# Performance work log

Measured on AMD Instinct MI355X. Metric: run time of the kernel, lower is better.

## Reference

```python
import jax, jax.numpy as jnp
import numpy as np
from jax import lax

EPS = 1e-12

def _l2norm(v, axis):
    n = jnp.linalg.norm(v, axis=axis, keepdims=True)
    return v / jnp.maximum(n, EPS)

def setup_inputs() -> dict:
    key = jax.random.key(0)
    k1, k2, k3 = jax.random.split(key, 3)
    C, H, W, K = 512, 192, 192, 64
    x = jax.random.normal(k1, (C, H, W), dtype=jnp.float32)
    conv_w = jax.random.normal(k2, (K, C), dtype=jnp.float32) * 0.05  # 1x1 conv, no bias (vladv2=False)
    centroids = jax.random.uniform(k3, (K, C), dtype=jnp.float32)
    return {"x": x, "conv_w": conv_w, "centroids": centroids}

def reference(x, conv_w, centroids):
    K = conv_w.shape[0]
    x4 = x[None]                      # [1,C,H,W]
    N, C, H, W = x4.shape
    L = H * W
    # descriptor-wise L2 normalization over channels
    x4 = _l2norm(x4, axis=1)
    # 1x1 conv -> soft assignment over clusters
    logits = jnp.einsum('kc,nchw->nkhw', conv_w, x4)
    soft = jax.nn.softmax(logits, axis=1)          # [N,K,H,W]
    sa_flat = soft.reshape(N, K, L)
    # top-2 cluster indices per location (argmax + second largest)
    _, top2 = lax.top_k(sa_flat.transpose(0, 2, 1), 2)  # [N,L,2]
    first, second = top2[..., 0], top2[..., 1]
    # unfold 3x3, padding 1: windows [N, L, K, 9] in (kh,kw) order
    pad = jnp.pad(soft, ((0, 0), (0, 0), (1, 1), (1, 1)))
    patches = jnp.stack([pad[:, :, di:di + H, dj:dj + W]
                         for di in range(3) for dj in range(3)], axis=2)  # [N,K,9,H,W]
    windows = patches.reshape(N, K, 9, L).transpose(0, 3, 1, 2)           # [N,L,K,9]
    # keep only windows of the top-2 clusters at each location
    karange = jnp.arange(K)[None, None, :]
    keep = (karange == first[:, :, None]) | (karange == second[:, :, None])  # [N,L,K]
    wsel = windows * keep[..., None].astype(windows.dtype)
    # fold (transpose of unfold): overlap-add back to [N,K,H,W]
    ws = wsel.transpose(0, 2, 3, 1).reshape(N, K, 9, H, W)
    out_pad = jnp.zeros((N, K, H + 2, W + 2), dtype=ws.dtype)
    t = 0
    for di in range(3):
        for dj in range(3):
            out_pad = out_pad.at[:, :, di:di + H, dj:dj + W].add(ws[:, :, t])
            t += 1
    weight = out_pad[:, :, 1:H + 1, 1:W + 1]
    # border mask: (min distance to border)^4
    ii = jnp.arange(H); jj = jnp.arange(W)
    mi = jnp.minimum(H - 1 - ii, ii)[:, None]
    mj = jnp.minimum(W - 1 - jj, jj)[None, :]
    m = jnp.minimum(mi, mj).astype(weight.dtype)
    m2 = m * m
    mask = m2 * m2
    weight = weight * mask[None, None]
    sa2 = weight.reshape(N, K, L)
    # per-cluster residual accumulation, vectorized (replaces the 64-iter loop)
    xf = x4.reshape(N, C, L)
    vlad = jnp.einsum('nkl,ncl->nkc', sa2, xf) - sa2.sum(-1)[..., None] * centroids[None]
    vlad = _l2norm(vlad, axis=2)               # intra-normalization
    v = vlad.reshape(N, -1)
    v = _l2norm(v, axis=1)
    return v
```

## Files before the change

kernel.cpp:

```cpp
#include <hip/hip_runtime.h>

#define HH 192
#define WW 192
#define LL (HH * WW)
#define CC 512
#define KK 64
#define EPSF 1e-12f
typedef unsigned long long ull;
typedef unsigned int uint;
typedef unsigned short ushort;

#define NCHUNK 192
#define CHUNKL (LL / NCHUNK)

typedef short bf16x8 __attribute__((ext_vector_type(8)));
typedef float f32x4 __attribute__((ext_vector_type(4)));

__global__ __launch_bounds__(256) void k0_transpose(const float* __restrict__ w,
                                                    float* __restrict__ wT,
                                                    float* __restrict__ Szero) {
    int idx = blockIdx.x * 256 + threadIdx.x;
    int k = idx >> 9;
    int c = idx & 511;
    wT[c * KK + k] = w[idx];
    if (blockIdx.x == 0 && threadIdx.x < 128) Szero[threadIdx.x] = 0.f;
}

__global__ __launch_bounds__(512) void k1_logits(const float* __restrict__ x,
                                                 const float* __restrict__ wT,
                                                 float* __restrict__ soft,
                                                 float* __restrict__ invn,
                                                 ull* __restrict__ keep) {
    __shared__ float accs[4][16][64];
    __shared__ float sss[64];
    __shared__ float sm1[4][64], sm2[4][64], ssum[4][64], sinv[64];
    __shared__ int   si1[4][64], si2[4][64];
    int t = threadIdx.x, lane = t & 63, wid = t >> 6;
    int l0 = blockIdx.x * 64;
    int kg = __builtin_amdgcn_readfirstlane((wid & 3) * 16);
    int ch = __builtin_amdgcn_readfirstlane((wid >> 2) * 256);

    const float* __restrict__ xcol = x + l0 + lane;

    float acc[16];
#pragma unroll
    for (int q = 0; q < 16; ++q) acc[q] = 0.f;
    float ss = 0.f;

    float xp[16], xn[16];
#pragma unroll
    for (int q = 0; q < 16; ++q) xp[q] = xcol[(size_t)(ch + q) * LL];

    for (int cb = ch; cb < ch + 256; cb += 16) {
        if (cb + 16 < ch + 256) {
#pragma unroll
            for (int q = 0; q < 16; ++q) xn[q] = xcol[(size_t)(cb + 16 + q) * LL];
        }
#pragma unroll
        for (int cc = 0; cc < 16; ++cc) {
            float xv = xp[cc];
            ss = fmaf(xv, xv, ss);
            const float* wr = wT + (size_t)(cb + cc) * KK + kg;
#pragma unroll
            for (int q = 0; q < 16; ++q) acc[q] = fmaf(wr[q], xv, acc[q]);
        }
        if (cb + 16 < ch + 256) {
#pragma unroll
            for (int q = 0; q < 16; ++q) xp[q] = xn[q];
        }
    }

    if (wid >= 4) {
        int w = wid - 4;
#pragma unroll
        for (int q = 0; q < 16; ++q) accs[w][q][lane] = acc[q];
        if (wid == 4) sss[lane] = ss;
    }
    __syncthreads();
    if (wid < 4) {
#pragma unroll
        for (int q = 0; q < 16; ++q) acc[q] += accs[wid][q][lane];
    }
    if (wid == 0) {
        ss += sss[lane];
        float iv = 1.0f / fmaxf(sqrtf(ss), EPSF);
        sinv[lane] = iv;
        invn[l0 + lane] = iv;
    }
    __syncthreads();
    float iv = sinv[lane];

    if (wid < 4) {
        float m1 = -3.0e38f, m2 = -3.0e38f; int i1 = 0, i2 = 0;
#pragma unroll
        for (int q = 0; q < 16; ++q) {
            float lg = acc[q] * iv;
            acc[q] = lg;
            if (lg > m1)      { m2 = m1; i2 = i1; m1 = lg; i1 = kg + q; }
            else if (lg > m2) { m2 = lg; i2 = kg + q; }
        }
        sm1[wid][lane] = m1; si1[wid][lane] = i1;
        sm2[wid][lane] = m2; si2[wid][lane] = i2;
    }
    __syncthreads();

    float M1 = -3.0e38f, M2 = -3.0e38f; int I1 = 0, I2 = 0;
    if (wid < 4) {
#pragma unroll
        for (int w2 = 0; w2 < 4; ++w2) {
            float a1 = sm1[w2][lane]; int b1 = si1[w2][lane];
            float a2 = sm2[w2][lane]; int b2 = si2[w2][lane];
            if (a1 > M1 || (a1 == M1 && b1 < I1)) { M2 = M1; I2 = I1; M1 = a1; I1 = b1; }
            else if (a1 > M2 || (a1 == M2 && b1 < I2)) { M2 = a1; I2 = b1; }
            if (a2 > M1 || (a2 == M1 && b2 < I1)) { M2 = M1; I2 = I1; M1 = a2; I1 = b2; }
            else if (a2 > M2 || (a2 == M2 && b2 < I2)) { M2 = a2; I2 = b2; }
        }
        float es = 0.f;
#pragma unroll
        for (int q = 0; q < 16; ++q) { float e = __expf(acc[q] - M1); acc[q] = e; es += e; }
        ssum[wid][lane] = es;
    }
    __syncthreads();
    if (wid < 4) {
        float St = ssum[0][lane] + ssum[1][lane] + ssum[2][lane] + ssum[3][lane];
        float rs = 1.0f / St;
        float4* sp = (float4*)(soft + (size_t)(l0 + lane) * KK + kg);
#pragma unroll
        for (int q4 = 0; q4 < 4; ++q4) {
            float4 v; v.x = acc[q4*4+0]*rs; v.y = acc[q4*4+1]*rs;
                      v.z = acc[q4*4+2]*rs; v.w = acc[q4*4+3]*rs;
            sp[q4] = v;
        }
        if (wid == 0) keep[l0 + lane] = (1ull << I1) | (1ull << I2);
    }
}

__global__ __launch_bounds__(256) void k2_weight(float* __restrict__ soft,
                                                 const ull* __restrict__ keep,
                                                 const float* __restrict__ invn,
                                                 float* __restrict__ S) {
    __shared__ float sred[4][64];
    int t = threadIdx.x, lane = t & 63, wid = t >> 6;
    int l0 = blockIdx.x * 32 + wid * 8;
    float sk = 0.f;
#pragma unroll
    for (int p = 0; p < 8; ++p) {
        int l = l0 + p;
        int i = l / WW, j = l % WW;
        int m = min(min(i, HH - 1 - i), min(j, WW - 1 - j));
        float bm = (float)m; bm *= bm; bm *= bm;
        int cnt = 0;
#pragma unroll
        for (int di = -1; di <= 1; ++di) {
            int ii = i + di;
            if (ii < 0 || ii >= HH) continue;
#pragma unroll
            for (int dj = -1; dj <= 1; ++dj) {
                int jj = j + dj;
                if (jj < 0 || jj >= WW) continue;
                ull nb = keep[ii * WW + jj];
                cnt += (int)((nb >> lane) & 1ull);
            }
        }
        float v = soft[(size_t)l * KK + lane];
        float u = v * (float)cnt * bm;
        sk += u;
        soft[(size_t)l * KK + lane] = u * invn[l];
    }
    sred[wid][lane] = sk;
    __syncthreads();
    if (wid == 0)
        atomicAdd(&S[lane], sred[0][lane] + sred[1][lane] + sred[2][lane] + sred[3][lane]);
}

__device__ inline void cvt_pair(float v0, float v1, uint& hp, uint& lp) {
    uint b0 = __float_as_uint(v0), b1 = __float_as_uint(v1);
    uint h0 = b0 & 0xFFFF0000u, h1 = b1 & 0xFFFF0000u;
    float r0 = v0 - __uint_as_float(h0);
    float r1 = v1 - __uint_as_float(h1);
    hp = (h0 >> 16) | h1;
    lp = (__float_as_uint(r0) >> 16) | (__float_as_uint(r1) & 0xFFFF0000u);
}

__global__ __launch_bounds__(256) void k3_mfma(const float* __restrict__ w2,
                                               const float* __restrict__ x,
                                               float* __restrict__ partials) {
    __shared__ ushort wa_hi[64][40], wa_lo[64][40];
    __shared__ ushort xb_hi[128][40], xb_lo[128][40];
    int chunk = blockIdx.x;
    int c0 = blockIdx.y * 128;
    int l0 = chunk * CHUNKL;
    int t = threadIdx.x, lane = t & 63, wid = t >> 6;
    int m = lane & 15, quad = lane >> 4;

    f32x4 acc[4][2];
#pragma unroll
    for (int kg = 0; kg < 4; ++kg)
#pragma unroll
        for (int cg = 0; cg < 2; ++cg) acc[kg][cg] = (f32x4){0.f, 0.f, 0.f, 0.f};

    for (int lb = 0; lb < CHUNKL; lb += 32) {
        {
            int k = t & 63, rg = t >> 6;
#pragma unroll
            for (int i = 0; i < 4; ++i) {
                int lp = rg + 4 * i;
                int gl = l0 + lb + 2 * lp;
                float v0 = w2[(size_t)gl * KK + k];
                float v1 = w2[(size_t)(gl + 1) * KK + k];
                uint hp, lq;
                cvt_pair(v0, v1, hp, lq);
                *(uint*)&wa_hi[k][2 * lp] = hp;
                *(uint*)&wa_lo[k][2 * lp] = lq;
            }
        }
        {
            int lp = t & 15, cb = t >> 4;
            int gl = l0 + lb + 2 * lp;
#pragma unroll
            for (int i = 0; i < 8; ++i) {
                int c = cb + 16 * i;
                float v0 = x[(size_t)(c0 + c) * LL + gl];
                float v1 = x[(size_t)(c0 + c) * LL + gl + 1];
                uint hp, lq;
                cvt_pair(v0, v1, hp, lq);
                *(uint*)&xb_hi[c][2 * lp] = hp;
                *(uint*)&xb_lo[c][2 * lp] = lq;
            }
        }
        __syncthreads();
        bf16x8 Ah[4], Al[4];
#pragma unroll
        for (int kg = 0; kg < 4; ++kg) {
            Ah[kg] = *(bf16x8*)&wa_hi[kg * 16 + m][quad * 8];
            Al[kg] = *(bf16x8*)&wa_lo[kg * 16 + m][quad * 8];
        }
#pragma unroll
        for (int cg = 0; cg < 2; ++cg) {
            int crow = wid * 32 + cg * 16 + m;
            bf16x8 Bh = *(bf16x8*)&xb_hi[crow][quad * 8];
            bf16x8 Bl = *(bf16x8*)&xb_lo[crow][quad * 8];
#pragma unroll
            for (int kg = 0; kg < 4; ++kg) {
                acc[kg][cg] = __builtin_amdgcn_mfma_f32_16x16x32_bf16(Ah[kg], Bh, acc[kg][cg], 0, 0, 0);
                acc[kg][cg] = __builtin_amdgcn_mfma_f32_16x16x32_bf16(Ah[kg], Bl, acc[kg][cg], 0, 0, 0);
                acc[kg][cg] = __builtin_amdgcn_mfma_f32_16x16x32_bf16(Al[kg], Bh, acc[kg][cg], 0, 0, 0);
            }
        }
        __syncthreads();
    }
    float* pp = partials + (size_t)chunk * KK * CC;
#pragma unroll
    for (int kg = 0; kg < 4; ++kg)
#pragma unroll
        for (int cg = 0; cg < 2; ++cg) {
            int cout = c0 + wid * 32 + cg * 16 + m;
#pragma unroll
            for (int r = 0; r < 4; ++r) {
                int kout = kg * 16 + quad * 4 + r;
                pp[(size_t)kout * CC + cout] = acc[kg][cg][r];
            }
        }
}

__global__ __launch_bounds__(512) void k4a_reduce(const float* __restrict__ partials,
                                                  const float* __restrict__ S,
                                                  const float* __restrict__ cent,
                                                  float* __restrict__ vlad,
                                                  float* __restrict__ rowsq) {
    __shared__ float red[512];
    int k = blockIdx.x;
    int ci = threadIdx.x & 127;
    int c = blockIdx.y * 128 + ci;
    int q = threadIdx.x >> 7;
    const float* pk = partials + (size_t)q * (NCHUNK / 4) * KK * CC + (size_t)k * CC + c;
    float s0 = 0.f, s1 = 0.f, s2 = 0.f, s3 = 0.f;
    for (int ch = 0; ch < NCHUNK / 4; ch += 4) {
        s0 += pk[(size_t)(ch + 0) * KK * CC];
        s1 += pk[(size_t)(ch + 1) * KK * CC];
        s2 += pk[(size_t)(ch + 2) * KK * CC];
        s3 += pk[(size_t)(ch + 3) * KK * CC];
    }
    red[threadIdx.x] = (s0 + s1) + (s2 + s3);
    __syncthreads();
    float vsq = 0.f;
    if (q == 0) {
        float v = red[ci] + red[ci + 128] + red[ci + 256] + red[ci + 384];
        v -= S[k] * cent[k * CC + c];
        vlad[k * CC + c] = v;
        vsq = v * v;
    }
    __syncthreads();
    red[threadIdx.x] = vsq;
    __syncthreads();
    for (int off = 256; off > 0; off >>= 1) {
        if (threadIdx.x < off) red[threadIdx.x] += red[threadIdx.x + off];
        __syncthreads();
    }
    if (threadIdx.x == 0) atomicAdd(&rowsq[k], red[0]);
}

__global__ __launch_bounds__(256) void k4c_finish(const float* __restrict__ vlad,
                                                  const float* __restrict__ rowsq,
                                                  float* __restrict__ out) {
    __shared__ float rns[64];
    int t = threadIdx.x;
    if (t < 64) {
        float tot = rowsq[t];
        float r = 1.0f / fmaxf(sqrtf(tot), EPSF);
        float contrib = tot * r * r;
#pragma unroll
        for (int off = 32; off; off >>= 1) contrib += __shfl_xor(contrib, off, 64);
        float ginv = 1.0f / fmaxf(sqrtf(contrib), EPSF);
        rns[t] = r * ginv;
    }
    __syncthreads();
    int idx4 = blockIdx.x * 256 + t;
    int k = idx4 >> 7;
    float s = rns[k];
    float4 v = ((const float4*)vlad)[idx4];
    v.x *= s; v.y *= s; v.z *= s; v.w *= s;
    ((float4*)out)[idx4] = v;
}

extern "C" void kernel_launch(void* const* d_in, const int* in_sizes, int n_in,
                              void* d_out, int out_size, void* d_ws, size_t ws_size,
                              hipStream_t stream) {
    const float* x      = (const float*)d_in[0];
    const float* conv_w = (const float*)d_in[1];
    const float* cent   = (const float*)d_in[2];
    float* out = (float*)d_out;

    float* ws    = (float*)d_ws;
    float* wT    = ws;
    float* soft  = wT + 32768;
    float* invn  = soft + (size_t)KK * LL;
    float* S     = invn + LL;
    float* rowsq = S + KK;
    float* vlad  = rowsq + KK;
    ull*   keep  = (ull*)(vlad + 32768);
    float* partials = (float*)(keep + LL);

    k0_transpose<<<(KK * CC) / 256, 256, 0, stream>>>(conv_w, wT, S);
    k1_logits<<<LL / 64, 512, 0, stream>>>(x, wT, soft, invn, keep);
    k2_weight<<<LL / 32, 256, 0, stream>>>(soft, keep, invn, S);
    k3_mfma<<<dim3(NCHUNK, 4), 256, 0, stream>>>(soft, x, partials);
    k4a_reduce<<<dim3(KK, 4), 512, 0, stream>>>(partials, S, cent, vlad, rowsq);
    k4c_finish<<<(KK * CC / 4) / 256, 256, 0, stream>>>(vlad, rowsq, out);
}
```

Before: 209.5 us.

## Compute logits with split-bf16 MFMA instead of scalar FP32 FMAs

Rewrites the logits kernel to use 16x16x32 bf16 MFMA instructions, splitting both the weights and x into three bf16 pieces and using six cross products to approximate FP32 accuracy. The weight prep kernel now pre-splits and reorders conv weights into an MFMA fragment layout. Top-2 selection, the norm and the softmax reductions now use cross-lane shuffles instead of shared memory with block syncs. This replaces a scalar-FMA-bound phase with matrix-core work, at the cost of extra split arithmetic on x and a small precision risk that could change top-2 tie outcomes.

```diff
diff --git a/kernel.cpp b/kernel.cpp
--- a/kernel.cpp
+++ b/kernel.cpp
@@ -16,122 +16,145 @@
 typedef short bf16x8 __attribute__((ext_vector_type(8)));
 typedef float f32x4 __attribute__((ext_vector_type(4)));
 
-__global__ __launch_bounds__(256) void k0_transpose(const float* __restrict__ w,
-                                                    float* __restrict__ wT,
-                                                    float* __restrict__ Szero) {
+__device__ inline void split3(float v, ushort& h, ushort& md, ushort& lo) {
+    uint b  = __float_as_uint(v);
+    uint hb = b & 0xFFFF0000u;
+    float r1 = v - __uint_as_float(hb);
+    uint mb = __float_as_uint(r1) & 0xFFFF0000u;
+    float r2 = r1 - __uint_as_float(mb);
+    uint lb = __float_as_uint(r2) & 0xFFFF0000u;
+    h = (ushort)(hb >> 16); md = (ushort)(mb >> 16); lo = (ushort)(lb >> 16);
+}
+
+__global__ __launch_bounds__(256) void k0_prep(const float* __restrict__ w,
+                                               ushort* __restrict__ Whi,
+                                               ushort* __restrict__ Wmid,
+                                               ushort* __restrict__ Wlo,
+                                               float* __restrict__ Szero) {
     int idx = blockIdx.x * 256 + threadIdx.x;
     int k = idx >> 9;
     int c = idx & 511;
-    wT[c * KK + k] = w[idx];
+    int s = c >> 5, w32 = c & 31, quad = w32 >> 3, j = w32 & 7;
+    int kg = k >> 4, m = k & 15;
+    int dst = (((s * 4 + kg) * 4 + quad) * 16 + m) * 8 + j;
+    float v = w[idx];
+    ushort h, md, lo;
+    split3(v, h, md, lo);
+    Whi[dst] = h; Wmid[dst] = md; Wlo[dst] = lo;
     if (blockIdx.x == 0 && threadIdx.x < 128) Szero[threadIdx.x] = 0.f;
 }
 
-__global__ __launch_bounds__(512) void k1_logits(const float* __restrict__ x,
-                                                 const float* __restrict__ wT,
+__global__ __launch_bounds__(128) void k1_logits(const float* __restrict__ x,
+                                                 const ushort* __restrict__ Whi,
+                                                 const ushort* __restrict__ Wmid,
+                                                 const ushort* __restrict__ Wlo,
                                                  float* __restrict__ soft,
                                                  float* __restrict__ invn,
                                                  ull* __restrict__ keep) {
-    __shared__ float accs[4][16][64];
-    __shared__ float sss[64];
-    __shared__ float sm1[4][64], sm2[4][64], ssum[4][64], sinv[64];
-    __shared__ int   si1[4][64], si2[4][64];
     int t = threadIdx.x, lane = t & 63, wid = t >> 6;
-    int l0 = blockIdx.x * 64;
-    int kg = __builtin_amdgcn_readfirstlane((wid & 3) * 16);
-    int ch = __builtin_amdgcn_readfirstlane((wid >> 2) * 256);
-
-    const float* __restrict__ xcol = x + l0 + lane;
-
-    float acc[16];
-#pragma unroll
-    for (int q = 0; q < 16; ++q) acc[q] = 0.f;
-    float ss = 0.f;
-
-    float xp[16], xn[16];
-#pragma unroll
-    for (int q = 0; q < 16; ++q) xp[q] = xcol[(size_t)(ch + q) * LL];
-
-    for (int cb = ch; cb < ch + 256; cb += 16) {
-        if (cb + 16 < ch + 256) {
-#pragma unroll
-            for (int q = 0; q < 16; ++q) xn[q] = xcol[(size_t)(cb + 16 + q) * LL];
-        }
-#pragma unroll
-        for (int cc = 0; cc < 16; ++cc) {
-            float xv = xp[cc];
-            ss = fmaf(xv, xv, ss);
-            const float* wr = wT + (size_t)(cb + cc) * KK + kg;
-#pragma unroll
-            for (int q = 0; q < 16; ++q) acc[q] = fmaf(wr[q], xv, acc[q]);
-        }
-        if (cb + 16 < ch + 256) {
-#pragma unroll
-            for (int q = 0; q < 16; ++q) xp[q] = xn[q];
-        }
-    }
-
-    if (wid >= 4) {
-        int w = wid - 4;
-#pragma unroll
-        for (int q = 0; q < 16; ++q) accs[w][q][lane] = acc[q];
-        if (wid == 4) sss[lane] = ss;
-    }
-    __syncthreads();
-    if (wid < 4) {
-#pragma unroll
-        for (int q = 0; q < 16; ++q) acc[q] += accs[wid][q][lane];
-    }
-    if (wid == 0) {
-        ss += sss[lane];
-        float iv = 1.0f / fmaxf(sqrtf(ss), EPSF);
-        sinv[lane] = iv;
-        invn[l0 + lane] = iv;
-    }
-    __syncthreads();
-    float iv = sinv[lane];
-
-    if (wid < 4) {
-        float m1 = -3.0e38f, m2 = -3.0e38f; int i1 = 0, i2 = 0;
-#pragma unroll
-        for (int q = 0; q < 16; ++q) {
-            float lg = acc[q] * iv;
-            acc[q] = lg;
-            if (lg > m1)      { m2 = m1; i2 = i1; m1 = lg; i1 = kg + q; }
-            else if (lg > m2) { m2 = lg; i2 = kg + q; }
-        }
-        sm1[wid][lane] = m1; si1[wid][lane] = i1;
-        sm2[wid][lane] = m2; si2[wid][lane] = i2;
-    }
-    __syncthreads();
-
-    float M1 = -3.0e38f, M2 = -3.0e38f; int I1 = 0, I2 = 0;
-    if (wid < 4) {
-#pragma unroll
-        for (int w2 = 0; w2 < 4; ++w2) {
-            float a1 = sm1[w2][lane]; int b1 = si1[w2][lane];
-            float a2 = sm2[w2][lane]; int b2 = si2[w2][lane];
+    int m = lane & 15, quad = lane >> 4;
+    int pb = blockIdx.x * 64 + wid * 32;
+
+    f32x4 acc[4][2];
+#pragma unroll
+    for (int kg = 0; kg < 4; ++kg)
+#pragma unroll
+        for (int cg = 0; cg < 2; ++cg) acc[kg][cg] = (f32x4){0.f, 0.f, 0.f, 0.f};
+    float ssA[2] = {0.f, 0.f};
+
+    const float* xq = x + (size_t)(quad * 8) * LL + pb + m;
+
+    for (int s = 0; s < 16; ++s) {
+        bf16x8 Ah[4], Am[4], Al[4];
+#pragma unroll
+        for (int kg = 0; kg < 4; ++kg) {
+            size_t off = (size_t)(((s * 4 + kg) * 64 + lane) * 8);
+            Ah[kg] = *(const bf16x8*)(Whi  + off);
+            Am[kg] = *(const bf16x8*)(Wmid + off);
+            Al[kg] = *(const bf16x8*)(Wlo  + off);
+        }
+        float xv[2][8];
+#pragma unroll
+        for (int j = 0; j < 8; ++j) {
+            const float* xr = xq + (size_t)j * LL;
+            xv[0][j] = xr[0];
+            xv[1][j] = xr[16];
+        }
+        xq += (size_t)32 * LL;
+        bf16x8 Bh[2], Bm[2], Bl[2];
+#pragma unroll
+        for (int cg = 0; cg < 2; ++cg)
+#pragma unroll
+            for (int j = 0; j < 8; ++j) {
+                float v = xv[cg][j];
+                ssA[cg] = fmaf(v, v, ssA[cg]);
+                ushort h, md, lo;
+                split3(v, h, md, lo);
+                Bh[cg][j] = (short)h; Bm[cg][j] = (short)md; Bl[cg][j] = (short)lo;
+            }
+#pragma unroll
+        for (int kg = 0; kg < 4; ++kg)
+#pragma unroll
+            for (int cg = 0; cg < 2; ++cg) {
+                f32x4 a = acc[kg][cg];
+                a = __builtin_amdgcn_mfma_f32_16x16x32_bf16(Ah[kg], Bh[cg], a, 0, 0, 0);
+                a = __builtin_amdgcn_mfma_f32_16x16x32_bf16(Ah[kg], Bm[cg], a, 0, 0, 0);
+                a = __builtin_amdgcn_mfma_f32_16x16x32_bf16(Am[kg], Bh[cg], a, 0, 0, 0);
+                a = __builtin_amdgcn_mfma_f32_16x16x32_bf16(Ah[kg], Bl[cg], a, 0, 0, 0);
+                a = __builtin_amdgcn_mfma_f32_16x16x32_bf16(Al[kg], Bh[cg], a, 0, 0, 0);
+                a = __builtin_amdgcn_mfma_f32_16x16x32_bf16(Am[kg], Bm[cg], a, 0, 0, 0);
+                acc[kg][cg] = a;
+            }
+    }
+
+#pragma unroll
+    for (int cg = 0; cg < 2; ++cg) {
+        float ssv = ssA[cg];
+        ssv += __shfl_xor(ssv, 16);
+        ssv += __shfl_xor(ssv, 32);
+        float iv = 1.0f / fmaxf(sqrtf(ssv), EPSF);
+        int px = pb + cg * 16 + m;
+        if (quad == 0) invn[px] = iv;
+
+        float lg[16];
+        float M1 = -3.0e38f, M2 = -3.0e38f; int I1 = 0, I2 = 0;
+#pragma unroll
+        for (int kg = 0; kg < 4; ++kg)
+#pragma unroll
+            for (int r = 0; r < 4; ++r) {
+                float v = acc[kg][cg][r] * iv;
+                lg[kg * 4 + r] = v;
+                int kk = kg * 16 + quad * 4 + r;
+                if (v > M1)      { M2 = M1; I2 = I1; M1 = v; I1 = kk; }
+                else if (v > M2) { M2 = v; I2 = kk; }
+            }
+#pragma unroll
+        for (int st = 0; st < 2; ++st) {
+            int d = 16 << st;
+            float a1 = __shfl_xor(M1, d); int b1 = __shfl_xor(I1, d);
+            float a2 = __shfl_xor(M2, d); int b2 = __shfl_xor(I2, d);
             if (a1 > M1 || (a1 == M1 && b1 < I1)) { M2 = M1; I2 = I1; M1 = a1; I1 = b1; }
             else if (a1 > M2 || (a1 == M2 && b1 < I2)) { M2 = a1; I2 = b1; }
             if (a2 > M1 || (a2 == M1 && b2 < I1)) { M2 = M1; I2 = I1; M1 = a2; I1 = b2; }
             else if (a2 > M2 || (a2 == M2 && b2 < I2)) { M2 = a2; I2 = b2; }
         }
+
         float es = 0.f;
 #pragma unroll
-        for (int q = 0; q < 16; ++q) { float e = __expf(acc[q] - M1); acc[q] = e; es += e; }
-        ssum[wid][lane] = es;
-    }
-    __syncthreads();
-    if (wid < 4) {
-        float St = ssum[0][lane] + ssum[1][lane] + ssum[2][lane] + ssum[3][lane];
-        float rs = 1.0f / St;
-        float4* sp = (float4*)(soft + (size_t)(l0 + lane) * KK + kg);
-#pragma unroll
-        for (int q4 = 0; q4 < 4; ++q4) {
-            float4 v; v.x = acc[q4*4+0]*rs; v.y = acc[q4*4+1]*rs;
-                      v.z = acc[q4*4+2]*rs; v.w = acc[q4*4+3]*rs;
-            sp[q4] = v;
-        }
-        if (wid == 0) keep[l0 + lane] = (1ull << I1) | (1ull << I2);
+        for (int q = 0; q < 16; ++q) { float e = __expf(lg[q] - M1); lg[q] = e; es += e; }
+        es += __shfl_xor(es, 16);
+        es += __shfl_xor(es, 32);
+        float rs = 1.0f / es;
+
+        float4* sp = (float4*)(soft + (size_t)px * KK + quad * 4);
+#pragma unroll
+        for (int kg = 0; kg < 4; ++kg) {
+            float4 o;
+            o.x = lg[kg * 4 + 0] * rs; o.y = lg[kg * 4 + 1] * rs;
+            o.z = lg[kg * 4 + 2] * rs; o.w = lg[kg * 4 + 3] * rs;
+            sp[kg * 4] = o;
+        }
+        if (quad == 0) keep[px] = (1ull << I1) | (1ull << I2);
     }
 }
 
@@ -332,8 +355,10 @@
     float* out = (float*)d_out;
 
     float* ws    = (float*)d_ws;
-    float* wT    = ws;
-    float* soft  = wT + 32768;
+    ushort* Whi  = (ushort*)ws;
+    ushort* Wmid = Whi + 32768;
+    ushort* Wlo  = Wmid + 32768;
+    float* soft  = ws + 49152;
     float* invn  = soft + (size_t)KK * LL;
     float* S     = invn + LL;
     float* rowsq = S + KK;
@@ -341,8 +366,8 @@
     ull*   keep  = (ull*)(vlad + 32768);
     float* partials = (float*)(keep + LL);
 
-    k0_transpose<<<(KK * CC) / 256, 256, 0, stream>>>(conv_w, wT, S);
-    k1_logits<<<LL / 64, 512, 0, stream>>>(x, wT, soft, invn, keep);
+    k0_prep<<<(KK * CC) / 256, 256, 0, stream>>>(conv_w, Whi, Wmid, Wlo, S);
+    k1_logits<<<LL / 64, 128, 0, stream>>>(x, Whi, Wmid, Wlo, soft, invn, keep);
     k2_weight<<<LL / 32, 256, 0, stream>>>(soft, keep, invn, S);
     k3_mfma<<<dim3(NCHUNK, 4), 256, 0, stream>>>(soft, x, partials);
     k4a_reduce<<<dim3(KK, 4), 512, 0, stream>>>(partials, S, cent, vlad, rowsq);
```

After: 203.0 us. 3.1% less time.
